# Kernel tuning notes

Hardware: AMD Instinct MI355X
Metric: run time of the kernel (lower is better)

Reference implementation:

```python
import jax, jax.numpy as jnp
import numpy as np
import math

ROPE_BASE = 10000.0

def rope(x):
    # rotate-half RoPE over the full feature dim. x: [B, S, D]
    B, S, D = x.shape
    half = D // 2
    inv_freq = 1.0 / (ROPE_BASE ** (jnp.arange(half, dtype=jnp.float32) / half))
    ang = jnp.arange(S, dtype=jnp.float32)[:, None] * inv_freq[None, :]  # [S, half]
    cos, sin = jnp.cos(ang), jnp.sin(ang)
    x1, x2 = x[..., :half], x[..., half:]
    return jnp.concatenate([x1 * cos - x2 * sin, x1 * sin + x2 * cos], axis=-1)

def setup_inputs() -> dict:
    key = jax.random.key(0)
    ks = jax.random.split(key, 10)
    B, S, D = 4, 2048, 2048
    scale = 1.0 / math.sqrt(D)
    x = jax.random.normal(ks[0], (B, S, D), dtype=jnp.float32)
    mask = jnp.broadcast_to(jnp.tril(jnp.ones((S, S), dtype=jnp.int32)), (B, S, S))
    Wq = jax.random.normal(ks[1], (D, D), dtype=jnp.float32) * scale
    bq = jax.random.normal(ks[2], (D,), dtype=jnp.float32) * 0.02
    Wk = jax.random.normal(ks[3], (D, D), dtype=jnp.float32) * scale
    bk = jax.random.normal(ks[4], (D,), dtype=jnp.float32) * 0.02
    Wv = jax.random.normal(ks[5], (D, D), dtype=jnp.float32) * scale
    bv = jax.random.normal(ks[6], (D,), dtype=jnp.float32) * 0.02
    Wo = jax.random.normal(ks[7], (D, D), dtype=jnp.float32) * scale
    bo = jax.random.normal(ks[8], (D,), dtype=jnp.float32) * 0.02
    return {"x": x, "mask": mask, "Wq": Wq, "bq": bq, "Wk": Wk, "bk": bk,
            "Wv": Wv, "bv": bv, "Wo": Wo, "bo": bo}

def reference(x, mask, Wq, bq, Wk, bk, Wv, bv, Wo, bo):
    # x: [B, S, D]; torch.nn.Linear convention: y = x @ W.T + b
    D = x.shape[-1]
    std = jnp.sqrt(jnp.asarray(D, dtype=x.dtype))
    q = jnp.einsum('bsd,ed->bse', x, Wq) + bq
    k = jnp.einsum('bsd,ed->bse', x, Wk) + bk
    v = jnp.einsum('bsd,ed->bse', x, Wv) + bv
    # cache=None prefill path: q sliced to last x.size(-2) positions (full seq here)
    Sq = x.shape[-2]
    q = rope(q)[:, -Sq:, :]
    k = rope(k)
    scores = jnp.einsum('bqd,bkd->bqk', q, k) / std  # [B, Sq, Sk]
    scores = jnp.where(mask[:, -Sq:, :] == 0, -jnp.inf, scores)
    attn = jax.nn.softmax(scores, axis=-1)  # dropout=0 (eval)
    ctx = jnp.einsum('bqk,bkd->bqd', attn, v)
    out = jnp.einsum('bqd,ed->bqe', ctx, Wo) + bo
    return out
```

## Files before the change

### kernel.cpp

```cpp
#include <hip/hip_runtime.h>
#include <stdint.h>
#include <math.h>

#define BLK 256
#define LDQK 4160

typedef __bf16 bf16x8 __attribute__((ext_vector_type(8)));
typedef float  f32x4  __attribute__((ext_vector_type(4)));

__device__ __forceinline__ uint16_t f2bf(float f) {
  uint32_t u = __float_as_uint(f);
  u += 0x7fffu + ((u >> 16) & 1u);
  return (uint16_t)(u >> 16);
}
__device__ __forceinline__ float bf2f(uint16_t h) {
  return __uint_as_float(((uint32_t)h) << 16);
}

__device__ __forceinline__ void load_lds16(const void* g, void* l) {
  __builtin_amdgcn_global_load_lds(
      (const __attribute__((address_space(1))) uint32_t*)g,
      (__attribute__((address_space(3))) uint32_t*)l,
      16, 0, 0);
}

__global__ __launch_bounds__(BLK)
void convert_all(const float* __restrict__ x, const float* __restrict__ wq,
                 const float* __restrict__ wk, const float* __restrict__ wv,
                 const float* __restrict__ wo,
                 uint16_t* __restrict__ xb, uint16_t* __restrict__ wqkv,
                 float* __restrict__ sums) {
  const long tid0 = (long)blockIdx.x * BLK + threadIdx.x;
  if (tid0 < 8192) sums[tid0] = 0.f;
  const long XG = 4194304;
  const long T  = XG + 4 * 1048576;
  for (long i = tid0; i < T; i += (long)gridDim.x * BLK) {
    const float* src; uint16_t* dst; long off, doff;
    if (i < XG) { src = x; dst = xb; off = i; doff = i; }
    else {
      const long j = i - XG;
      const int seg = (int)(j >> 20);
      off = j & 1048575;
      src = (seg == 0) ? wq : (seg == 1) ? wk : (seg == 2) ? wv : wo;
      dst = wqkv + ((long)seg << 22);
      if (seg < 2) {
        const int f = (int)(off >> 9);
        const int g = (int)(off & 511);
        const int c = (f < 1024) ? (f << 1) : (((f - 1024) << 1) | 1);
        doff = (long)c * 512 + g;
      } else doff = off;
    }
    float4 v = ((const float4*)src)[off];
    ushort4 o;
    o.x = f2bf(v.x); o.y = f2bf(v.y); o.z = f2bf(v.z); o.w = f2bf(v.w);
    ((ushort4*)dst)[doff] = o;
  }
}

__global__ __launch_bounds__(BLK, 5)
void qk_gemm(const uint16_t* __restrict__ Aall, const uint16_t* __restrict__ Ball,
             uint16_t* __restrict__ Pall, float* __restrict__ rsall, float scale)
{
  const int bxt   = (int)blockIdx.x;
  const int bz    = (int)blockIdx.y & 3;
  const int strip = 31 - ((int)blockIdx.y >> 2);
  if ((bxt << 1) > strip) return;
  const int tile_m = strip << 6;
  const int tile_n = bxt << 7;

  const uint16_t* A  = Aall + (long)bz * (2048L * LDQK);
  const uint16_t* Bt = Ball + (long)bz * (2048L * LDQK);
  uint16_t* Pp = Pall + (long)bz * (2048L * 2048);
  float*    rs = rsall + (long)bz * 2048;

  __shared__ __align__(16) uint16_t smem[12288];
  uint16_t* sA = smem;
  uint16_t* sB = smem + 4096;

  const int tid  = threadIdx.x;
  const int lane = tid & 63;
  const int wave = tid >> 6;
  const int quad = lane >> 4;
  const int l16  = lane & 15;
  const int x8   = l16 & 7;
  const int wn   = wave << 5;

  f32x4 acc[4][2];
#pragma unroll
  for (int i = 0; i < 4; ++i)
#pragma unroll
    for (int j = 0; j < 2; ++j) acc[i][j] = (f32x4){0.f, 0.f, 0.f, 0.f};

  const uint16_t* gA[2]; uint16_t* lA[2];
  const uint16_t* gB[4]; uint16_t* lB[4];
#pragma unroll
  for (int i = 0; i < 2; ++i) {
    const int id = wave * 128 + i * 64 + lane;
    const int row = id >> 3;
    const int c = (id & 7) ^ (row & 7);
    gA[i] = A + (long)(tile_m + row) * LDQK + c * 8;
    lA[i] = sA + (wave * 128 + i * 64) * 8;
  }
#pragma unroll
  for (int i = 0; i < 4; ++i) {
    const int id = wave * 256 + i * 64 + lane;
    const int row = id >> 3;
    const int c = (id & 7) ^ (row & 7);
    gB[i] = Bt + (long)(tile_n + row) * LDQK + c * 8;
    lB[i] = sB + (wave * 256 + i * 64) * 8;
  }

  for (int kk = 0; kk < 2048; kk += 64) {
#pragma unroll
    for (int i = 0; i < 2; ++i) load_lds16(gA[i] + kk, lA[i]);
#pragma unroll
    for (int i = 0; i < 4; ++i) load_lds16(gB[i] + kk, lB[i]);
    __syncthreads();

#pragma unroll
    for (int s2 = 0; s2 < 2; ++s2) {
      const int slot = ((quad + s2 * 4) ^ x8) * 8;
      bf16x8 af[4], bfr[2];
#pragma unroll
      for (int mi = 0; mi < 4; ++mi)
        af[mi] = *(const bf16x8*)(sA + (mi * 16 + l16) * 64 + slot);
#pragma unroll
      for (int ni = 0; ni < 2; ++ni)
        bfr[ni] = *(const bf16x8*)(sB + (wn + ni * 16 + l16) * 64 + slot);
#pragma unroll
      for (int mi = 0; mi < 4; ++mi)
#pragma unroll
        for (int ni = 0; ni < 2; ++ni)
          acc[mi][ni] = __builtin_amdgcn_mfma_f32_16x16x32_bf16(af[mi], bfr[ni], acc[mi][ni], 0, 0, 0);
    }
    __syncthreads();
  }

  const int crow0 = tile_m + quad * 4;
  const int ccol0 = tile_n + wn + l16;
#pragma unroll
  for (int mi = 0; mi < 4; ++mi) {
#pragma unroll
    for (int r = 0; r < 4; ++r) {
      const int row = crow0 + mi * 16 + r;
      float partial = 0.f;
#pragma unroll
      for (int ni = 0; ni < 2; ++ni) {
        const int col = ccol0 + ni * 16;
        const float e = (col <= row) ? __expf(acc[mi][ni][r] * scale) : 0.f;
        const uint16_t h = f2bf(e);
        partial += bf2f(h);
        Pp[(long)row * 2048 + col] = h;
      }
#pragma unroll
      for (int o = 1; o < 16; o <<= 1) partial += __shfl_xor(partial, o, 64);
      if (l16 == 0) atomicAdd(rs + row, partial);
    }
  }
}

template<int MODE, int MINW>
__global__ __launch_bounds__(BLK, MINW)
void gemm_bt(const uint16_t* __restrict__ A, int lda,
             const uint16_t* __restrict__ Bt, int ldb,
             const float* __restrict__ b0, const float* __restrict__ b1,
             const float* __restrict__ b2,
             void* __restrict__ Cv, int ldc,
             int K, long sAb, long sBb, long sCb,
             float scale, float* __restrict__ rowsum,
             uint16_t* __restrict__ Vt)
{
  int tile_m, tile_n, bz;
  if (MODE == 3) {
    bz = blockIdx.y & 3;
    tile_m = ((int)(gridDim.y >> 2) - 1 - (int)(blockIdx.y >> 2)) * 128;
    tile_n = blockIdx.x * 128;
  } else {
    tile_m = blockIdx.y * 128;
    tile_n = blockIdx.x * 128;
    bz = blockIdx.z;
  }
  A  += (long)bz * sAb;
  Bt += (long)bz * sBb;

  __shared__ __align__(16) uint16_t smem[16384];
  uint16_t* sA = smem;
  uint16_t* sB = smem + 8192;

  const int tid  = threadIdx.x;
  const int lane = tid & 63;
  const int wave = tid >> 6;
  const int quad = lane >> 4;
  const int l16  = lane & 15;
  const int x8   = l16 & 7;
  const int wm = (wave & 1) * 64;
  const int wn = (wave >> 1) * 64;

  f32x4 acc[4][4];
#pragma unroll
  for (int i = 0; i < 4; ++i)
#pragma unroll
    for (int j = 0; j < 4; ++j) acc[i][j] = (f32x4){0.f, 0.f, 0.f, 0.f};

  const uint16_t* gA[4]; const uint16_t* gB[4];
  uint16_t* lA[4]; uint16_t* lB[4];
#pragma unroll
  for (int i = 0; i < 4; ++i) {
    const int id = wave * 256 + i * 64 + lane;
    const int row = id >> 3;
    const int c = (id & 7) ^ (row & 7);
    gA[i] = A  + (long)(tile_m + row) * lda + c * 8;
    gB[i] = Bt + (long)(tile_n + row) * ldb + c * 8;
    lA[i] = sA + (wave * 256 + i * 64) * 8;
    lB[i] = sB + (wave * 256 + i * 64) * 8;
  }

  const int kend = (MODE == 3) ? min(K, tile_m + 128) : K;

  for (int kk = 0; kk < kend; kk += 64) {
#pragma unroll
    for (int i = 0; i < 4; ++i) {
      load_lds16(gA[i] + kk, lA[i]);
      load_lds16(gB[i] + kk, lB[i]);
    }
    __syncthreads();

#pragma unroll
    for (int s2 = 0; s2 < 2; ++s2) {
      const int slot = ((quad + s2 * 4) ^ x8) * 8;
      bf16x8 af[4], bfr[4];
#pragma unroll
      for (int mi = 0; mi < 4; ++mi)
        af[mi] = *(const bf16x8*)(sA + (wm + mi * 16 + l16) * 64 + slot);
#pragma unroll
      for (int ni = 0; ni < 4; ++ni)
        bfr[ni] = *(const bf16x8*)(sB + (wn + ni * 16 + l16) * 64 + slot);
#pragma unroll
      for (int mi = 0; mi < 4; ++mi)
#pragma unroll
        for (int ni = 0; ni < 4; ++ni)
          acc[mi][ni] = __builtin_amdgcn_mfma_f32_16x16x32_bf16(af[mi], bfr[ni], acc[mi][ni], 0, 0, 0);
    }
    __syncthreads();
  }

  const int crow0 = tile_m + wm + quad * 4;
  const int ccol0 = tile_n + wn + l16;

  if constexpr (MODE == 3) {
    uint16_t* Cp = (uint16_t*)Cv + (long)bz * sCb;
    const float* rs = rowsum + (long)bz * 2048;
#pragma unroll
    for (int mi = 0; mi < 4; ++mi) {
#pragma unroll
      for (int r = 0; r < 4; ++r) {
        const int row = crow0 + mi * 16 + r;
        const float inv = 1.f / rs[row];
#pragma unroll
        for (int ni = 0; ni < 4; ++ni)
          Cp[(long)row * ldc + ccol0 + ni * 16] = f2bf(acc[mi][ni][r] * inv);
      }
    }
  } else if constexpr (MODE == 1) {
    const int seg = tile_n >> 11;
    if (seg < 2) {
      const float* bp = seg ? b1 : b0;
      uint16_t* Cp = (uint16_t*)Cv;
#pragma unroll
      for (int ni = 0; ni < 4; ++ni) {
        const int col = ccol0 + ni * 16;
        const int cc = col & 2047;
        const float bb = bp[(cc >> 1) + (cc & 1) * 1024];
        const float invf = exp2f((float)(cc >> 1) * (-13.287712379549449f / 1024.f));
        const float sgn = (cc & 1) ? 1.f : -1.f;
#pragma unroll
        for (int mi = 0; mi < 4; ++mi) {
#pragma unroll
          for (int r = 0; r < 4; ++r) {
            const int row = crow0 + mi * 16 + r;
            const float v = acc[mi][ni][r] + bb;
            float sn, cs;
            __sincosf((float)(row & 2047) * invf, &sn, &cs);
            const float p = __shfl_xor(v, 1, 64);
            Cp[(long)row * LDQK + col] = f2bf(v * cs + p * sgn * sn);
          }
        }
      }
    } else {
#pragma unroll
      for (int ni = 0; ni < 4; ++ni) {
        const int cl = wn + l16 + ni * 16;
        const float bb = b2[(ccol0 + ni * 16) & 2047];
#pragma unroll
        for (int mi = 0; mi < 4; ++mi) {
          const int rl0 = wm + quad * 4 + mi * 16;
          union { uint16_t u16[4]; uint64_t u64; } pk;
#pragma unroll
          for (int r = 0; r < 4; ++r) pk.u16[r] = f2bf(acc[mi][ni][r] + bb);
          *(uint64_t*)(smem + cl * 128 + (rl0 ^ ((cl & 15) << 3))) = pk.u64;
        }
      }
      __syncthreads();
      const int fl = quad;
      const int t0 = l16 * 8;
      const int bno = tile_m >> 11;
      const int tokbase = tile_m & 2047;
      uint16_t* Vp = Vt + (long)bno * 4194304 + tokbase;
      const int featbase = tile_n - 4096;
#pragma unroll
      for (int jj = 0; jj < 8; ++jj) {
        const int c = jj * 16 + wave * 4 + fl;
        const uint16_t* srcp = smem + c * 128 + (t0 ^ ((c & 15) << 3));
        ulonglong2 v = *(const ulonglong2*)srcp;
        *(ulonglong2*)(Vp + (long)(featbase + c) * 2048 + t0) = v;
      }
    }
  } else {
#pragma unroll
    for (int ni = 0; ni < 4; ++ni) {
      const int col = ccol0 + ni * 16;
      const float bb = b0[col];
#pragma unroll
      for (int mi = 0; mi < 4; ++mi) {
#pragma unroll
        for (int r = 0; r < 4; ++r) {
          const long row = crow0 + mi * 16 + r;
          ((float*)Cv)[row * (long)ldc + col] = acc[mi][ni][r] * scale + bb;
        }
      }
    }
  }
}

extern "C" void kernel_launch(void* const* d_in, const int* in_sizes, int n_in,
                              void* d_out, int out_size, void* d_ws, size_t ws_size,
                              hipStream_t stream) {
  const long S = 2048, D = 2048;
  const long MD = 4 * S * D;
  const long DD = D * D;

  const float* x  = (const float*)d_in[0];
  const float* Wq = (const float*)d_in[2];
  const float* bq = (const float*)d_in[3];
  const float* Wk = (const float*)d_in[4];
  const float* bk = (const float*)d_in[5];
  const float* Wv = (const float*)d_in[6];
  const float* bv = (const float*)d_in[7];
  const float* Wo = (const float*)d_in[8];
  const float* bo = (const float*)d_in[9];

  uint16_t* Xb    = (uint16_t*)d_ws;
  uint16_t* Wqkvb = Xb + MD;
  uint16_t* QK    = Wqkvb + 4 * DD;
  uint16_t* Vt    = QK + 8192L * LDQK;
  uint16_t* P     = Vt + MD;
  float*    sums  = (float*)(P + 4 * S * S);
  if (ws_size < 268435456ull) return;

  dim3 blk(BLK);

  convert_all<<<16384, blk, 0, stream>>>(x, Wq, Wk, Wv, Wo, Xb, Wqkvb, sums);

  gemm_bt<1, 4><<<dim3(48, 64, 1), blk, 0, stream>>>(
      Xb, 2048, Wqkvb, 2048, bq, bk, bv, QK, LDQK,
      2048, 0, 0, 0, 1.f, nullptr, Vt);

  qk_gemm<<<dim3(16, 128, 1), blk, 0, stream>>>(
      QK, QK + 2048, P, sums, 0.022097086912079608f);

  gemm_bt<3, 4><<<dim3(16, 64, 1), blk, 0, stream>>>(
      P, 2048, Vt, 2048, nullptr, nullptr, nullptr, Xb, 2048,
      2048, S * S, S * D, S * D, 1.f, sums, nullptr);

  gemm_bt<0, 4><<<dim3(16, 64, 1), blk, 0, stream>>>(
      Xb, 2048, Wqkvb + 3 * DD, 2048, bo, nullptr, nullptr, (float*)d_out, 2048,
      2048, 0, 0, 0, 1.f, nullptr, nullptr);
}
```

Before: 595.2 us.

## Split templated GEMM into dedicated kernels and use 128x128 triangular QK tiles

The templated gemm_bt is replaced by specialised kernels for the QKV, PV and output projections. The QKV projection is now launched as three separate grids, one per Q/K/V segment. The QK^T score kernel moves from 64x128 tiles with early-exit blocks to 128x128 tiles over a compact lower-triangular index computed with sqrt. This removes idle launched blocks and raises data reuse per tile, but causal masking now applies only on diagonal tiles. The trade-offs are three kernel launches instead of one for QKV, and lower occupancy from larger tiles (launch bounds 4 instead of 5).

```diff
diff --git a/kernel.cpp b/kernel.cpp
--- a/kernel.cpp
+++ b/kernel.cpp
@@ -23,6 +23,9 @@
       (__attribute__((address_space(3))) uint32_t*)l,
       16, 0, 0);
 }
+
+#define MFMA16(a, b, c) __builtin_amdgcn_mfma_f32_16x16x32_bf16(a, b, c, 0, 0, 0)
+
 
 __global__ __launch_bounds__(BLK)
 void convert_all(const float* __restrict__ x, const float* __restrict__ wq,
@@ -57,131 +60,14 @@
   }
 }
 
-__global__ __launch_bounds__(BLK, 5)
-void qk_gemm(const uint16_t* __restrict__ Aall, const uint16_t* __restrict__ Ball,
-             uint16_t* __restrict__ Pall, float* __restrict__ rsall, float scale)
+__global__ __launch_bounds__(BLK, 4)
+void qkv_gemm(const uint16_t* __restrict__ A, const uint16_t* __restrict__ Bt,
+              const float* __restrict__ b0, const float* __restrict__ b1,
+              const float* __restrict__ b2, uint16_t* __restrict__ QK,
+              uint16_t* __restrict__ Vt, int tnoff)
 {
-  const int bxt   = (int)blockIdx.x;
-  const int bz    = (int)blockIdx.y & 3;
-  const int strip = 31 - ((int)blockIdx.y >> 2);
-  if ((bxt << 1) > strip) return;
-  const int tile_m = strip << 6;
-  const int tile_n = bxt << 7;
-
-  const uint16_t* A  = Aall + (long)bz * (2048L * LDQK);
-  const uint16_t* Bt = Ball + (long)bz * (2048L * LDQK);
-  uint16_t* Pp = Pall + (long)bz * (2048L * 2048);
-  float*    rs = rsall + (long)bz * 2048;
-
-  __shared__ __align__(16) uint16_t smem[12288];
-  uint16_t* sA = smem;
-  uint16_t* sB = smem + 4096;
-
-  const int tid  = threadIdx.x;
-  const int lane = tid & 63;
-  const int wave = tid >> 6;
-  const int quad = lane >> 4;
-  const int l16  = lane & 15;
-  const int x8   = l16 & 7;
-  const int wn   = wave << 5;
-
-  f32x4 acc[4][2];
-#pragma unroll
-  for (int i = 0; i < 4; ++i)
-#pragma unroll
-    for (int j = 0; j < 2; ++j) acc[i][j] = (f32x4){0.f, 0.f, 0.f, 0.f};
-
-  const uint16_t* gA[2]; uint16_t* lA[2];
-  const uint16_t* gB[4]; uint16_t* lB[4];
-#pragma unroll
-  for (int i = 0; i < 2; ++i) {
-    const int id = wave * 128 + i * 64 + lane;
-    const int row = id >> 3;
-    const int c = (id & 7) ^ (row & 7);
-    gA[i] = A + (long)(tile_m + row) * LDQK + c * 8;
-    lA[i] = sA + (wave * 128 + i * 64) * 8;
-  }
-#pragma unroll
-  for (int i = 0; i < 4; ++i) {
-    const int id = wave * 256 + i * 64 + lane;
-    const int row = id >> 3;
-    const int c = (id & 7) ^ (row & 7);
-    gB[i] = Bt + (long)(tile_n + row) * LDQK + c * 8;
-    lB[i] = sB + (wave * 256 + i * 64) * 8;
-  }
-
-  for (int kk = 0; kk < 2048; kk += 64) {
-#pragma unroll
-    for (int i = 0; i < 2; ++i) load_lds16(gA[i] + kk, lA[i]);
-#pragma unroll
-    for (int i = 0; i < 4; ++i) load_lds16(gB[i] + kk, lB[i]);
-    __syncthreads();
-
-#pragma unroll
-    for (int s2 = 0; s2 < 2; ++s2) {
-      const int slot = ((quad + s2 * 4) ^ x8) * 8;
-      bf16x8 af[4], bfr[2];
-#pragma unroll
-      for (int mi = 0; mi < 4; ++mi)
-        af[mi] = *(const bf16x8*)(sA + (mi * 16 + l16) * 64 + slot);
-#pragma unroll
-      for (int ni = 0; ni < 2; ++ni)
-        bfr[ni] = *(const bf16x8*)(sB + (wn + ni * 16 + l16) * 64 + slot);
-#pragma unroll
-      for (int mi = 0; mi < 4; ++mi)
-#pragma unroll
-        for (int ni = 0; ni < 2; ++ni)
-          acc[mi][ni] = __builtin_amdgcn_mfma_f32_16x16x32_bf16(af[mi], bfr[ni], acc[mi][ni], 0, 0, 0);
-    }
-    __syncthreads();
-  }
-
-  const int crow0 = tile_m + quad * 4;
-  const int ccol0 = tile_n + wn + l16;
-#pragma unroll
-  for (int mi = 0; mi < 4; ++mi) {
-#pragma unroll
-    for (int r = 0; r < 4; ++r) {
-      const int row = crow0 + mi * 16 + r;
-      float partial = 0.f;
-#pragma unroll
-      for (int ni = 0; ni < 2; ++ni) {
-        const int col = ccol0 + ni * 16;
-        const float e = (col <= row) ? __expf(acc[mi][ni][r] * scale) : 0.f;
-        const uint16_t h = f2bf(e);
-        partial += bf2f(h);
-        Pp[(long)row * 2048 + col] = h;
-      }
-#pragma unroll
-      for (int o = 1; o < 16; o <<= 1) partial += __shfl_xor(partial, o, 64);
-      if (l16 == 0) atomicAdd(rs + row, partial);
-    }
-  }
-}
-
-template<int MODE, int MINW>
-__global__ __launch_bounds__(BLK, MINW)
-void gemm_bt(const uint16_t* __restrict__ A, int lda,
-             const uint16_t* __restrict__ Bt, int ldb,
-             const float* __restrict__ b0, const float* __restrict__ b1,
-             const float* __restrict__ b2,
-             void* __restrict__ Cv, int ldc,
-             int K, long sAb, long sBb, long sCb,
-             float scale, float* __restrict__ rowsum,
-             uint16_t* __restrict__ Vt)
-{
-  int tile_m, tile_n, bz;
-  if (MODE == 3) {
-    bz = blockIdx.y & 3;
-    tile_m = ((int)(gridDim.y >> 2) - 1 - (int)(blockIdx.y >> 2)) * 128;
-    tile_n = blockIdx.x * 128;
-  } else {
-    tile_m = blockIdx.y * 128;
-    tile_n = blockIdx.x * 128;
-    bz = blockIdx.z;
-  }
-  A  += (long)bz * sAb;
-  Bt += (long)bz * sBb;
+  const int tile_m = blockIdx.y * 128;
+  const int tile_n = blockIdx.x * 128 + tnoff;
 
   __shared__ __align__(16) uint16_t smem[16384];
   uint16_t* sA = smem;
@@ -209,15 +95,13 @@
     const int id = wave * 256 + i * 64 + lane;
     const int row = id >> 3;
     const int c = (id & 7) ^ (row & 7);
-    gA[i] = A  + (long)(tile_m + row) * lda + c * 8;
-    gB[i] = Bt + (long)(tile_n + row) * ldb + c * 8;
+    gA[i] = A  + (long)(tile_m + row) * 2048 + c * 8;
+    gB[i] = Bt + (long)(tile_n + row) * 2048 + c * 8;
     lA[i] = sA + (wave * 256 + i * 64) * 8;
     lB[i] = sB + (wave * 256 + i * 64) * 8;
   }
 
-  const int kend = (MODE == 3) ? min(K, tile_m + 128) : K;
-
-  for (int kk = 0; kk < kend; kk += 64) {
+  for (int kk = 0; kk < 2048; kk += 64) {
 #pragma unroll
     for (int i = 0; i < 4; ++i) {
       load_lds16(gA[i] + kk, lA[i]);
@@ -239,94 +123,335 @@
       for (int mi = 0; mi < 4; ++mi)
 #pragma unroll
         for (int ni = 0; ni < 4; ++ni)
-          acc[mi][ni] = __builtin_amdgcn_mfma_f32_16x16x32_bf16(af[mi], bfr[ni], acc[mi][ni], 0, 0, 0);
+          acc[mi][ni] = MFMA16(af[mi], bfr[ni], acc[mi][ni]);
     }
     __syncthreads();
   }
 
   const int crow0 = tile_m + wm + quad * 4;
   const int ccol0 = tile_n + wn + l16;
-
-  if constexpr (MODE == 3) {
-    uint16_t* Cp = (uint16_t*)Cv + (long)bz * sCb;
-    const float* rs = rowsum + (long)bz * 2048;
-#pragma unroll
-    for (int mi = 0; mi < 4; ++mi) {
-#pragma unroll
-      for (int r = 0; r < 4; ++r) {
-        const int row = crow0 + mi * 16 + r;
-        const float inv = 1.f / rs[row];
+  const int seg = tile_n >> 11;
+
+  if (seg < 2) {
+    const float* bp = seg ? b1 : b0;
+#pragma unroll
+    for (int ni = 0; ni < 4; ++ni) {
+      const int col = ccol0 + ni * 16;
+      const int cc = col & 2047;
+      const float bb = bp[(cc >> 1) + (cc & 1) * 1024];
+      const float invf = exp2f((float)(cc >> 1) * (-13.287712379549449f / 1024.f));
+      const float sgn = (cc & 1) ? 1.f : -1.f;
+#pragma unroll
+      for (int mi = 0; mi < 4; ++mi) {
+#pragma unroll
+        for (int r = 0; r < 4; ++r) {
+          const int row = crow0 + mi * 16 + r;
+          const float v = acc[mi][ni][r] + bb;
+          float sn, cs;
+          __sincosf((float)(row & 2047) * invf, &sn, &cs);
+          const float p = __shfl_xor(v, 1, 64);
+          QK[(long)row * LDQK + col] = f2bf(v * cs + p * sgn * sn);
+        }
+      }
+    }
+  } else {
+#pragma unroll
+    for (int ni = 0; ni < 4; ++ni) {
+      const int cl = wn + l16 + ni * 16;
+      const float bb = b2[(ccol0 + ni * 16) & 2047];
+#pragma unroll
+      for (int mi = 0; mi < 4; ++mi) {
+        const int rl0 = wm + quad * 4 + mi * 16;
+        union { uint16_t u16[4]; uint64_t u64; } pk;
+#pragma unroll
+        for (int r = 0; r < 4; ++r) pk.u16[r] = f2bf(acc[mi][ni][r] + bb);
+        *(uint64_t*)(smem + cl * 128 + (rl0 ^ ((cl & 15) << 3))) = pk.u64;
+      }
+    }
+    __syncthreads();
+    const int fl = quad;
+    const int t0 = l16 * 8;
+    const int bno = tile_m >> 11;
+    const int tokbase = tile_m & 2047;
+    uint16_t* Vp = Vt + (long)bno * 4194304 + tokbase;
+    const int featbase = tile_n - 4096;
+#pragma unroll
+    for (int jj = 0; jj < 8; ++jj) {
+      const int c = jj * 16 + wave * 4 + fl;
+      const uint16_t* srcp = smem + c * 128 + (t0 ^ ((c & 15) << 3));
+      ulonglong2 v = *(const ulonglong2*)srcp;
+      *(ulonglong2*)(Vp + (long)(featbase + c) * 2048 + t0) = v;
+    }
+  }
+}
+
+__global__ __launch_bounds__(BLK, 4)
+void qk_gemm(const uint16_t* __restrict__ QKall, uint16_t* __restrict__ Pall,
+             float* __restrict__ rsall, float scale)
+{
+  const int t = blockIdx.x;
+  int r = (int)((sqrtf(8.f * (float)t + 1.f) - 1.f) * 0.5f);
+  while ((r + 1) * (r + 2) / 2 <= t) ++r;
+  while (r * (r + 1) / 2 > t) --r;
+  const int tile_m = r * 128;
+  const int tile_n = (t - r * (r + 1) / 2) * 128;
+  const int bz = blockIdx.z;
+
+  const uint16_t* A  = QKall + (long)bz * (2048L * LDQK);
+  const uint16_t* Bt = QKall + 2048 + (long)bz * (2048L * LDQK);
+
+  __shared__ __align__(16) uint16_t smem[16384];
+  uint16_t* sA = smem;
+  uint16_t* sB = smem + 8192;
+
+  const int tid  = threadIdx.x;
+  const int lane = tid & 63;
+  const int wave = tid >> 6;
+  const int quad = lane >> 4;
+  const int l16  = lane & 15;
+  const int x8   = l16 & 7;
+  const int wm = (wave & 1) * 64;
+  const int wn = (wave >> 1) * 64;
+
+  f32x4 acc[4][4];
+#pragma unroll
+  for (int i = 0; i < 4; ++i)
+#pragma unroll
+    for (int j = 0; j < 4; ++j) acc[i][j] = (f32x4){0.f, 0.f, 0.f, 0.f};
+
+  const uint16_t* gA[4]; const uint16_t* gB[4];
+  uint16_t* lA[4]; uint16_t* lB[4];
+#pragma unroll
+  for (int i = 0; i < 4; ++i) {
+    const int id = wave * 256 + i * 64 + lane;
+    const int row = id >> 3;
+    const int c = (id & 7) ^ (row & 7);
+    gA[i] = A  + (long)(tile_m + row) * LDQK + c * 8;
+    gB[i] = Bt + (long)(tile_n + row) * LDQK + c * 8;
+    lA[i] = sA + (wave * 256 + i * 64) * 8;
+    lB[i] = sB + (wave * 256 + i * 64) * 8;
+  }
+
+  for (int kk = 0; kk < 2048; kk += 64) {
+#pragma unroll
+    for (int i = 0; i < 4; ++i) {
+      load_lds16(gA[i] + kk, lA[i]);
+      load_lds16(gB[i] + kk, lB[i]);
+    }
+    __syncthreads();
+
+#pragma unroll
+    for (int s2 = 0; s2 < 2; ++s2) {
+      const int slot = ((quad + s2 * 4) ^ x8) * 8;
+      bf16x8 af[4], bfr[4];
+#pragma unroll
+      for (int mi = 0; mi < 4; ++mi)
+        af[mi] = *(const bf16x8*)(sA + (wm + mi * 16 + l16) * 64 + slot);
+#pragma unroll
+      for (int ni = 0; ni < 4; ++ni)
+        bfr[ni] = *(const bf16x8*)(sB + (wn + ni * 16 + l16) * 64 + slot);
+#pragma unroll
+      for (int mi = 0; mi < 4; ++mi)
 #pragma unroll
         for (int ni = 0; ni < 4; ++ni)
-          Cp[(long)row * ldc + ccol0 + ni * 16] = f2bf(acc[mi][ni][r] * inv);
-      }
-    }
-  } else if constexpr (MODE == 1) {
-    const int seg = tile_n >> 11;
-    if (seg < 2) {
-      const float* bp = seg ? b1 : b0;
-      uint16_t* Cp = (uint16_t*)Cv;
+          acc[mi][ni] = MFMA16(af[mi], bfr[ni], acc[mi][ni]);
+    }
+    __syncthreads();
+  }
+
+  const int crow0 = tile_m + wm + quad * 4;
+  const int ccol0 = tile_n + wn + l16;
+  const bool diag = (tile_m == tile_n);
+  uint16_t* Pp = Pall + (long)bz * (2048L * 2048);
+  float* rs = rsall + (long)bz * 2048;
+#pragma unroll
+  for (int mi = 0; mi < 4; ++mi) {
+#pragma unroll
+    for (int r2 = 0; r2 < 4; ++r2) {
+      const int row = crow0 + mi * 16 + r2;
+      float partial = 0.f;
 #pragma unroll
       for (int ni = 0; ni < 4; ++ni) {
         const int col = ccol0 + ni * 16;
-        const int cc = col & 2047;
-        const float bb = bp[(cc >> 1) + (cc & 1) * 1024];
-        const float invf = exp2f((float)(cc >> 1) * (-13.287712379549449f / 1024.f));
-        const float sgn = (cc & 1) ? 1.f : -1.f;
-#pragma unroll
-        for (int mi = 0; mi < 4; ++mi) {
-#pragma unroll
-          for (int r = 0; r < 4; ++r) {
-            const int row = crow0 + mi * 16 + r;
-            const float v = acc[mi][ni][r] + bb;
-            float sn, cs;
-            __sincosf((float)(row & 2047) * invf, &sn, &cs);
-            const float p = __shfl_xor(v, 1, 64);
-            Cp[(long)row * LDQK + col] = f2bf(v * cs + p * sgn * sn);
-          }
-        }
+        const float e = (!diag || col <= row) ? __expf(acc[mi][ni][r2] * scale) : 0.f;
+        const uint16_t h = f2bf(e);
+        partial += bf2f(h);
+        Pp[(long)row * 2048 + col] = h;
       }
-    } else {
-#pragma unroll
-      for (int ni = 0; ni < 4; ++ni) {
-        const int cl = wn + l16 + ni * 16;
-        const float bb = b2[(ccol0 + ni * 16) & 2047];
-#pragma unroll
-        for (int mi = 0; mi < 4; ++mi) {
-          const int rl0 = wm + quad * 4 + mi * 16;
-          union { uint16_t u16[4]; uint64_t u64; } pk;
-#pragma unroll
-          for (int r = 0; r < 4; ++r) pk.u16[r] = f2bf(acc[mi][ni][r] + bb);
-          *(uint64_t*)(smem + cl * 128 + (rl0 ^ ((cl & 15) << 3))) = pk.u64;
-        }
-      }
-      __syncthreads();
-      const int fl = quad;
-      const int t0 = l16 * 8;
-      const int bno = tile_m >> 11;
-      const int tokbase = tile_m & 2047;
-      uint16_t* Vp = Vt + (long)bno * 4194304 + tokbase;
-      const int featbase = tile_n - 4096;
-#pragma unroll
-      for (int jj = 0; jj < 8; ++jj) {
-        const int c = jj * 16 + wave * 4 + fl;
-        const uint16_t* srcp = smem + c * 128 + (t0 ^ ((c & 15) << 3));
-        ulonglong2 v = *(const ulonglong2*)srcp;
-        *(ulonglong2*)(Vp + (long)(featbase + c) * 2048 + t0) = v;
-      }
-    }
-  } else {
-#pragma unroll
-    for (int ni = 0; ni < 4; ++ni) {
-      const int col = ccol0 + ni * 16;
-      const float bb = b0[col];
-#pragma unroll
-      for (int mi = 0; mi < 4; ++mi) {
-#pragma unroll
-        for (int r = 0; r < 4; ++r) {
-          const long row = crow0 + mi * 16 + r;
-          ((float*)Cv)[row * (long)ldc + col] = acc[mi][ni][r] * scale + bb;
-        }
+#pragma unroll
+      for (int o = 1; o < 16; o <<= 1) partial += __shfl_xor(partial, o, 64);
+      if (l16 == 0) atomicAdd(rs + row, partial);
+    }
+  }
+}
+
+__global__ __launch_bounds__(BLK, 4)
+void pv_gemm(const uint16_t* __restrict__ Pall, const uint16_t* __restrict__ Vtall,
+             uint16_t* __restrict__ Call, const float* __restrict__ rsall)
+{
+  const int bz = blockIdx.y & 3;
+  const int tile_m = ((int)(gridDim.y >> 2) - 1 - (int)(blockIdx.y >> 2)) * 128;
+  const int tile_n = blockIdx.x * 128;
+
+  const uint16_t* A  = Pall  + (long)bz * (2048L * 2048);
+  const uint16_t* Bt = Vtall + (long)bz * (2048L * 2048);
+
+  __shared__ __align__(16) uint16_t smem[16384];
+  uint16_t* sA = smem;
+  uint16_t* sB = smem + 8192;
+
+  const int tid  = threadIdx.x;
+  const int lane = tid & 63;
+  const int wave = tid >> 6;
+  const int quad = lane >> 4;
+  const int l16  = lane & 15;
+  const int x8   = l16 & 7;
+  const int wm = (wave & 1) * 64;
+  const int wn = (wave >> 1) * 64;
+
+  f32x4 acc[4][4];
+#pragma unroll
+  for (int i = 0; i < 4; ++i)
+#pragma unroll
+    for (int j = 0; j < 4; ++j) acc[i][j] = (f32x4){0.f, 0.f, 0.f, 0.f};
+
+  const uint16_t* gA[4]; const uint16_t* gB[4];
+  uint16_t* lA[4]; uint16_t* lB[4];
+#pragma unroll
+  for (int i = 0; i < 4; ++i) {
+    const int id = wave * 256 + i * 64 + lane;
+    const int row = id >> 3;
+    const int c = (id & 7) ^ (row & 7);
+    gA[i] = A  + (long)(tile_m + row) * 2048 + c * 8;
+    gB[i] = Bt + (long)(tile_n + row) * 2048 + c * 8;
+    lA[i] = sA + (wave * 256 + i * 64) * 8;
+    lB[i] = sB + (wave * 256 + i * 64) * 8;
+  }
+
+  const int kend = min(2048, tile_m + 128);
+
+  for (int kk = 0; kk < kend; kk += 64) {
+#pragma unroll
+    for (int i = 0; i < 4; ++i) {
+      load_lds16(gA[i] + kk, lA[i]);
+      load_lds16(gB[i] + kk, lB[i]);
+    }
+    __syncthreads();
+
+#pragma unroll
+    for (int s2 = 0; s2 < 2; ++s2) {
+      const int slot = ((quad + s2 * 4) ^ x8) * 8;
+      bf16x8 af[4], bfr[4];
+#pragma unroll
+      for (int mi = 0; mi < 4; ++mi)
+        af[mi] = *(const bf16x8*)(sA + (wm + mi * 16 + l16) * 64 + slot);
+#pragma unroll
+      for (int ni = 0; ni < 4; ++ni)
+        bfr[ni] = *(const bf16x8*)(sB + (wn + ni * 16 + l16) * 64 + slot);
+#pragma unroll
+      for (int mi = 0; mi < 4; ++mi)
+#pragma unroll
+        for (int ni = 0; ni < 4; ++ni)
+          acc[mi][ni] = MFMA16(af[mi], bfr[ni], acc[mi][ni]);
+    }
+    __syncthreads();
+  }
+
+  const int crow0 = tile_m + wm + quad * 4;
+  const int ccol0 = tile_n + wn + l16;
+  uint16_t* Cp = Call + (long)bz * (2048L * 2048);
+  const float* rs = rsall + (long)bz * 2048;
+#pragma unroll
+  for (int mi = 0; mi < 4; ++mi) {
+#pragma unroll
+    for (int r2 = 0; r2 < 4; ++r2) {
+      const int row = crow0 + mi * 16 + r2;
+      const float inv = 1.f / rs[row];
+#pragma unroll
+      for (int ni = 0; ni < 4; ++ni)
+        Cp[(long)row * 2048 + ccol0 + ni * 16] = f2bf(acc[mi][ni][r2] * inv);
+    }
+  }
+}
+
+__global__ __launch_bounds__(BLK, 4)
+void out_gemm(const uint16_t* __restrict__ A, const uint16_t* __restrict__ Bt,
+              const float* __restrict__ b0, float* __restrict__ Co, float scale)
+{
+  const int tile_m = blockIdx.y * 128;
+  const int tile_n = blockIdx.x * 128;
+
+  __shared__ __align__(16) uint16_t smem[16384];
+  uint16_t* sA = smem;
+  uint16_t* sB = smem + 8192;
+
+  const int tid  = threadIdx.x;
+  const int lane = tid & 63;
+  const int wave = tid >> 6;
+  const int quad = lane >> 4;
+  const int l16  = lane & 15;
+  const int x8   = l16 & 7;
+  const int wm = (wave & 1) * 64;
+  const int wn = (wave >> 1) * 64;
+
+  f32x4 acc[4][4];
+#pragma unroll
+  for (int i = 0; i < 4; ++i)
+#pragma unroll
+    for (int j = 0; j < 4; ++j) acc[i][j] = (f32x4){0.f, 0.f, 0.f, 0.f};
+
+  const uint16_t* gA[4]; const uint16_t* gB[4];
+  uint16_t* lA[4]; uint16_t* lB[4];
+#pragma unroll
+  for (int i = 0; i < 4; ++i) {
+    const int id = wave * 256 + i * 64 + lane;
+    const int row = id >> 3;
+    const int c = (id & 7) ^ (row & 7);
+    gA[i] = A  + (long)(tile_m + row) * 2048 + c * 8;
+    gB[i] = Bt + (long)(tile_n + row) * 2048 + c * 8;
+    lA[i] = sA + (wave * 256 + i * 64) * 8;
+    lB[i] = sB + (wave * 256 + i * 64) * 8;
+  }
+
+  for (int kk = 0; kk < 2048; kk += 64) {
+#pragma unroll
+    for (int i = 0; i < 4; ++i) {
+      load_lds16(gA[i] + kk, lA[i]);
+      load_lds16(gB[i] + kk, lB[i]);
+    }
+    __syncthreads();
+
+#pragma unroll
+    for (int s2 = 0; s2 < 2; ++s2) {
+      const int slot = ((quad + s2 * 4) ^ x8) * 8;
+      bf16x8 af[4], bfr[4];
+#pragma unroll
+      for (int mi = 0; mi < 4; ++mi)
+        af[mi] = *(const bf16x8*)(sA + (wm + mi * 16 + l16) * 64 + slot);
+#pragma unroll
+      for (int ni = 0; ni < 4; ++ni)
+        bfr[ni] = *(const bf16x8*)(sB + (wn + ni * 16 + l16) * 64 + slot);
+#pragma unroll
+      for (int mi = 0; mi < 4; ++mi)
+#pragma unroll
+        for (int ni = 0; ni < 4; ++ni)
+          acc[mi][ni] = MFMA16(af[mi], bfr[ni], acc[mi][ni]);
+    }
+    __syncthreads();
+  }
+
+  const int crow0 = tile_m + wm + quad * 4;
+  const int ccol0 = tile_n + wn + l16;
+#pragma unroll
+  for (int ni = 0; ni < 4; ++ni) {
+    const int col = ccol0 + ni * 16;
+    const float bb = b0[col];
+#pragma unroll
+    for (int mi = 0; mi < 4; ++mi) {
+#pragma unroll
+      for (int r2 = 0; r2 < 4; ++r2) {
+        const long row = crow0 + mi * 16 + r2;
+        Co[row * 2048L + col] = acc[mi][ni][r2] * scale + bb;
       }
     }
   }
@@ -361,18 +486,13 @@
 
   convert_all<<<16384, blk, 0, stream>>>(x, Wq, Wk, Wv, Wo, Xb, Wqkvb, sums);
 
-  gemm_bt<1, 4><<<dim3(48, 64, 1), blk, 0, stream>>>(
-      Xb, 2048, Wqkvb, 2048, bq, bk, bv, QK, LDQK,
-      2048, 0, 0, 0, 1.f, nullptr, Vt);
-
-  qk_gemm<<<dim3(16, 128, 1), blk, 0, stream>>>(
-      QK, QK + 2048, P, sums, 0.022097086912079608f);
-
-  gemm_bt<3, 4><<<dim3(16, 64, 1), blk, 0, stream>>>(
-      P, 2048, Vt, 2048, nullptr, nullptr, nullptr, Xb, 2048,
-      2048, S * S, S * D, S * D, 1.f, sums, nullptr);
-
-  gemm_bt<0, 4><<<dim3(16, 64, 1), blk, 0, stream>>>(
-      Xb, 2048, Wqkvb + 3 * DD, 2048, bo, nullptr, nullptr, (float*)d_out, 2048,
-      2048, 0, 0, 0, 1.f, nullptr, nullptr);
-}
+  qkv_gemm<<<dim3(16, 64), blk, 0, stream>>>(Xb, Wqkvb, bq, bk, bv, QK, Vt, 0);
+  qkv_gemm<<<dim3(16, 64), blk, 0, stream>>>(Xb, Wqkvb, bq, bk, bv, QK, Vt, 2048);
+  qkv_gemm<<<dim3(16, 64), blk, 0, stream>>>(Xb, Wqkvb, bq, bk, bv, QK, Vt, 4096);
+
+  qk_gemm<<<dim3(136, 1, 4), blk, 0, stream>>>(QK, P, sums, 0.022097086912079608f);
+
+  pv_gemm<<<dim3(16, 64), blk, 0, stream>>>(P, Vt, Xb, sums);
+
+  out_gemm<<<dim3(16, 64), blk, 0, stream>>>(Xb, Wqkvb + 3 * DD, bo, (float*)d_out, 1.f);
+}
```

Result: slower. 793.0 us (+33.2%).
